# Optimization experiments

Hardware: AMD Instinct MI355X
Metric: run time of the kernel (lower is better)

## Reference

```python
import jax, jax.numpy as jnp
import numpy as np

N = 50000          # nodes
E_RAND = 600000    # random edges (self-loops appended -> E = 650000)
H, C = 2, 128      # heads, per-head channels
IN, OUT = 128, 40
SLOPE = 0.2        # PyG GATv2 default negative_slope
EPS = 1e-16


def setup_inputs() -> dict:
    key = jax.random.key(0)
    ks = jax.random.split(key, 16)
    x = jax.random.normal(ks[0], (N, IN), jnp.float32)
    src = jax.random.randint(ks[1], (E_RAND,), 0, N)
    dst = jax.random.randint(ks[2], (E_RAND,), 0, N)
    loops = jnp.arange(N)
    edge_index = jnp.stack([jnp.concatenate([src, loops]),
                            jnp.concatenate([dst, loops])]).astype(jnp.int64)

    def glorot(k, shape):
        fan = shape[0] + shape[-1]
        return jax.random.normal(k, shape, jnp.float32) * jnp.sqrt(2.0 / fan)

    return {
        "x": x, "edge_index": edge_index,
        "Wl1": glorot(ks[3], (IN, H * C)), "Wr1": glorot(ks[4], (IN, H * C)),
        "att1": glorot(ks[5], (H, C)), "b1": jnp.zeros((H * C,), jnp.float32),
        "Wl2": glorot(ks[6], (H * C, H * C)), "Wr2": glorot(ks[7], (H * C, H * C)),
        "att2": glorot(ks[8], (H, C)), "b2": jnp.zeros((H * C,), jnp.float32),
        "W3": glorot(ks[9], (H * C, C)), "b3": jnp.zeros((C,), jnp.float32),
        "W4": glorot(ks[10], (C, OUT)), "b4": jnp.zeros((OUT,), jnp.float32),
    }


def gatv2_conv(x, src, dst, Wl, Wr, att, b):
    # x: [N, F]; lin_l -> source messages, lin_r -> target. Output concat heads.
    xl = (x @ Wl).reshape(-1, H, C)              # [N,H,C]
    xr = (x @ Wr).reshape(-1, H, C)
    e = jax.nn.leaky_relu(xl[src] + xr[dst], SLOPE)   # [E,H,C]
    score = jnp.einsum('ehc,hc->eh', e, att)          # [E,H]
    # segment softmax over incoming edges of each dst node
    m = jax.ops.segment_max(score, dst, num_segments=N)       # [N,H]
    a = jnp.exp(score - m[dst])
    denom = jax.ops.segment_sum(a, dst, num_segments=N)
    alpha = a / (denom[dst] + EPS)                              # [E,H]
    out = jax.ops.segment_sum(alpha[:, :, None] * xl[src], dst, num_segments=N)
    return out.reshape(-1, H * C) + b


def reference(x, edge_index, Wl1, Wr1, att1, b1, Wl2, Wr2, att2, b2, W3, b3, W4, b4):
    src, dst = edge_index[0], edge_index[1]
    h = jax.nn.relu(gatv2_conv(x, src, dst, Wl1, Wr1, att1, b1))   # dropout: eval mode
    h = jax.nn.relu(gatv2_conv(h, src, dst, Wl2, Wr2, att2, b2))
    h = h @ W3 + b3
    h = h @ W4 + b4
    return jax.nn.sigmoid(h)   # [N, OUT]
```

## Files before the change

kernel.cpp:

```cpp
#include <hip/hip_runtime.h>
#include <hip/hip_bf16.h>
#include <math.h>

typedef __attribute__((ext_vector_type(4))) float f32x4;
typedef __attribute__((ext_vector_type(8))) short s16x8;
typedef __attribute__((ext_vector_type(8))) unsigned short u16x8;

#define CAP 48

__device__ inline unsigned short f2b(float f) {
    union { float f; unsigned u; } x; x.f = f;
    unsigned r = x.u + 0x7FFF + ((x.u >> 16) & 1);
    return (unsigned short)(r >> 16);
}
__device__ inline float b2f(unsigned short b) {
    union { unsigned u; float f; } x; x.u = ((unsigned)b) << 16; return x.f;
}

__device__ inline void gload_lds16(const void* g, void* l) {
    __builtin_amdgcn_global_load_lds(
        (const __attribute__((address_space(1))) void*)g,
        (__attribute__((address_space(3))) void*)l, 16, 0, 0);
}

#define GBM 128
#define GBN 256
#define GBK 64

__global__ __launch_bounds__(512) void gemm_mfma(
    const unsigned short* __restrict__ A, const unsigned short* __restrict__ Bt,
    const float* __restrict__ bias, void* __restrict__ Cout, void* __restrict__ Cout2,
    int M, int Nn, int K, int split, int mode)
{
    __shared__ unsigned short As[GBM * GBK];
    __shared__ unsigned short Bs[GBN * GBK];
    const int tid = threadIdx.x;
    const int lane = tid & 63;
    const int w = tid >> 6, wm = w >> 2, wn = w & 3;
    const int row0 = blockIdx.y * GBM, col0 = blockIdx.x * GBN;
    const int l15 = lane & 15, l7 = lane & 7, lhi = lane >> 4;

    f32x4 acc[4][4] = {};

    for (int k0 = 0; k0 < K; k0 += GBK) {
        #pragma unroll
        for (int i = 0; i < 2; i++) {
            int L = i * 512 + tid;
            int row = L >> 3;
            int c = (L & 7) ^ (row & 7);
            int gr = row0 + row; gr = gr < M ? gr : M - 1;
            gload_lds16(A + (size_t)gr * K + k0 + c * 8, (char*)As + L * 16);
        }
        #pragma unroll
        for (int i = 0; i < 4; i++) {
            int L = i * 512 + tid;
            int row = L >> 3;
            int c = (L & 7) ^ (row & 7);
            gload_lds16(Bt + (size_t)(col0 + row) * K + k0 + c * 8, (char*)Bs + L * 16);
        }
        __syncthreads();
        #pragma unroll
        for (int kk = 0; kk < 2; kk++) {
            s16x8 af[4], bf[4];
            #pragma unroll
            for (int i = 0; i < 4; i++) {
                int slot = (wm * 64 + i * 16 + l15) * 8 + ((kk * 4 + lhi) ^ l7);
                af[i] = *(const s16x8*)((const char*)As + slot * 16);
            }
            #pragma unroll
            for (int j = 0; j < 4; j++) {
                int slot = (wn * 64 + j * 16 + l15) * 8 + ((kk * 4 + lhi) ^ l7);
                bf[j] = *(const s16x8*)((const char*)Bs + slot * 16);
            }
            #pragma unroll
            for (int i = 0; i < 4; i++)
                #pragma unroll
                for (int j = 0; j < 4; j++)
                    acc[i][j] = __builtin_amdgcn_mfma_f32_16x16x32_bf16(
                        af[i], bf[j], acc[i][j], 0, 0, 0);
        }
        __syncthreads();
    }

    if (mode == 0) {
        unsigned short* C  = (unsigned short*)Cout;
        unsigned short* C2 = (unsigned short*)Cout2;
        const int ld2 = Nn - split;
        #pragma unroll
        for (int i = 0; i < 4; i++)
            #pragma unroll
            for (int r = 0; r < 4; r++) {
                int row = row0 + wm * 64 + i * 16 + lhi * 4 + r;
                if (row >= M) continue;
                #pragma unroll
                for (int j = 0; j < 4; j++) {
                    int col = col0 + wn * 64 + j * 16 + l15;
                    unsigned short val = f2b(acc[i][j][r]);
                    if (col < split) C[(size_t)row * split + col] = val;
                    else             C2[(size_t)row * ld2 + (col - split)] = val;
                }
            }
    } else {
        float* C = (float*)Cout;
        #pragma unroll
        for (int i = 0; i < 4; i++)
            #pragma unroll
            for (int r = 0; r < 4; r++) {
                int row = row0 + wm * 64 + i * 16 + lhi * 4 + r;
                if (row >= M) continue;
                #pragma unroll
                for (int j = 0; j < 4; j++) {
                    int col = col0 + wn * 64 + j * 16 + l15;
                    if (col >= split) continue;
                    float v = acc[i][j][r] + bias[col];
                    C[(size_t)row * split + col] = 1.f / (1.f + __expf(-v));
                }
            }
    }
}

#define PA 6250
#define PB 6282
#define PC 6346
#define PE 6602

__global__ __launch_bounds__(256) void k_prep(
    const float* __restrict__ x,
    const float* __restrict__ Wl1, const float* __restrict__ Wr1,
    const float* __restrict__ Wl2, const float* __restrict__ Wr2,
    const float* __restrict__ W3,  const float* __restrict__ W4,
    const float* __restrict__ b3,  const float* __restrict__ b4,
    unsigned short* __restrict__ xbf,
    unsigned short* __restrict__ Wcat1, unsigned short* __restrict__ Wcat2,
    unsigned short* __restrict__ W34t, float* __restrict__ b34)
{
    __shared__ float w4c[128];
    const int b = blockIdx.x, tid = threadIdx.x;

    if (b < PA) {
        int i = b * 1024 + tid * 4;
        float4 v = *(const float4*)&x[i];
        ushort4 o = { f2b(v.x), f2b(v.y), f2b(v.z), f2b(v.w) };
        *(ushort4*)&xbf[i] = o;
    } else if (b < PB) {
        int base = (b - PA) * 2048 + tid * 8;
        #pragma unroll
        for (int j = 0; j < 8; j++) {
            int e = base + j;
            int ep = e & 32767, n = ep >> 7, k = ep & 127;
            const float* srcp = (e < 32768) ? Wl1 : Wr1;
            Wcat1[e] = f2b(srcp[k * 256 + n]);
        }
    } else if (b < PC) {
        int base = (b - PB) * 2048 + tid * 8;
        #pragma unroll
        for (int j = 0; j < 8; j++) {
            int e = base + j;
            int ep = e & 65535, n = ep >> 8, k = ep & 255;
            const float* srcp = (e < 65536) ? Wl2 : Wr2;
            Wcat2[e] = f2b(srcp[k * 256 + n]);
        }
    } else {
        int n = b - PC;
        if (n < 40) {
            if (tid < 128) w4c[tid] = W4[tid * 40 + n];
            __syncthreads();
            float s = 0.f;
            const float4* p = (const float4*)&W3[(size_t)tid * 128];
            #pragma unroll
            for (int j = 0; j < 32; j++) {
                float4 v = p[j];
                s = fmaf(v.x, w4c[j * 4 + 0], s);
                s = fmaf(v.y, w4c[j * 4 + 1], s);
                s = fmaf(v.z, w4c[j * 4 + 2], s);
                s = fmaf(v.w, w4c[j * 4 + 3], s);
            }
            W34t[(size_t)n * 256 + tid] = f2b(s);
            if (tid == 0) {
                float t = b4[n];
                for (int j = 0; j < 128; j++) t = fmaf(b3[j], w4c[j], t);
                b34[n] = t;
            }
        } else {
            W34t[(size_t)n * 256 + tid] = 0;
        }
    }
}

__global__ void k_fillb(const int* __restrict__ src, const int* __restrict__ dstv, int E,
    int* __restrict__ cnt, int* __restrict__ colA)
{
    int e = blockIdx.x * blockDim.x + threadIdx.x;
    if (e >= E) return;
    int d = dstv[e];
    int slot = atomicAdd(&cnt[d], 1);
    colA[d * CAP + slot] = src[e] << 8;
}

__global__ __launch_bounds__(256) void k_attn(const unsigned short* __restrict__ xl,
    const unsigned short* __restrict__ xr, const float* __restrict__ att,
    const int* __restrict__ cnt, const int* __restrict__ colA,
    const float* __restrict__ bias, int Nn, unsigned short* __restrict__ outp)
{
    int n = blockIdx.x * 4 + (threadIdx.x >> 6);
    int lane = threadIdx.x & 63;
    if (n >= Nn) return;
    const int lh = lane & 31;
    const int h  = lane >> 5;
    int r0 = n * CAP;
    int r1 = r0 + cnt[n];

    const float LOG2E = 1.4426950408889634f;
    u16x8 xb = *(const u16x8*)&xr[(size_t)n * 256 + lh * 8];
    float xrv[8], w[8];
    #pragma unroll
    for (int k = 0; k < 8; k++) { xrv[k] = b2f(xb[k]); w[k] = att[lh * 8 + k] * LOG2E; }

    float m = -INFINITY, l = 0.f;
    float acc[8] = {};

    auto update = [&](const u16x8& vb) {
        float v[8];
        #pragma unroll
        for (int k = 0; k < 8; k++) v[k] = b2f(vb[k]);
        float dot = 0.f;
        #pragma unroll
        for (int k = 0; k < 8; k++) {
            float t = v[k] + xrv[k];
            t = fmaxf(t, 0.2f * t);
            dot = fmaf(t, w[k], dot);
        }
        #pragma unroll
        for (int off = 1; off <= 8; off <<= 1) dot += __shfl_xor(dot, off);
        if (__ballot(dot > m + 8.f)) {
            float mn = fmaxf(m, dot);
            float sc = exp2f(m - mn);
            float we = exp2f(dot - mn);
            l = l * sc + we;
            #pragma unroll
            for (int k = 0; k < 8; k++) acc[k] = acc[k] * sc + we * v[k];
            m = mn;
        } else {
            float we = exp2f(dot - m);
            l += we;
            #pragma unroll
            for (int k = 0; k < 8; k++) acc[k] = fmaf(we, v[k], acc[k]);
        }
    };

    int s = r0 + h;
    for (; s + 2 < r1; s += 4) {
        int c0 = colA[s], c1 = colA[s + 2];
        u16x8 v0 = *(const u16x8*)&xl[(size_t)c0 + lh * 8];
        u16x8 v1 = *(const u16x8*)&xl[(size_t)c1 + lh * 8];
        update(v0);
        update(v1);
    }
    for (; s < r1; s += 2) {
        int c = colA[s];
        u16x8 v = *(const u16x8*)&xl[(size_t)c + lh * 8];
        update(v);
    }

    float mq = (m == -INFINITY) ? -1e30f : m;
    float mo = __shfl_xor(mq, 32);
    float lo = __shfl_xor(l, 32);
    float ms = fmaxf(mq, mo);
    float es = exp2f(mq - ms), eo = exp2f(mo - ms);
    float lt = l * es + lo * eo + 1e-16f;
    float inv = 1.f / lt;

    u16x8 o;
    #pragma unroll
    for (int k = 0; k < 8; k++) {
        float other = __shfl_xor(acc[k], 32);
        float r = (acc[k] * es + other * eo) * inv + bias[lh * 8 + k];
        o[k] = f2b(fmaxf(r, 0.f));
    }
    if (h == 0) *(u16x8*)&outp[(size_t)n * 256 + lh * 8] = o;
}

extern "C" void kernel_launch(void* const* d_in, const int* in_sizes, int n_in,
                              void* d_out, int out_size, void* d_ws, size_t ws_size,
                              hipStream_t stream)
{
    const float* x    = (const float*)d_in[0];
    const int*   ei   = (const int*)d_in[1];
    const float* Wl1  = (const float*)d_in[2];
    const float* Wr1  = (const float*)d_in[3];
    const float* att1 = (const float*)d_in[4];
    const float* b1   = (const float*)d_in[5];
    const float* Wl2  = (const float*)d_in[6];
    const float* Wr2  = (const float*)d_in[7];
    const float* att2 = (const float*)d_in[8];
    const float* b2   = (const float*)d_in[9];
    const float* W3   = (const float*)d_in[10];
    const float* b3   = (const float*)d_in[11];
    const float* W4   = (const float*)d_in[12];
    const float* b4   = (const float*)d_in[13];

    const int N = in_sizes[0] / 128;
    const int E = in_sizes[1] / 2;
    const int* src  = ei;
    const int* dstv = ei + E;
    float* out = (float*)d_out;

    char* ws = (char*)d_ws;
    size_t o = 0;
    auto alloc = [&](size_t bytes) -> void* {
        void* p = ws + o;
        o += (bytes + 255) & ~(size_t)255;
        return p;
    };
    unsigned short* xbf    = (unsigned short*)alloc((size_t)N * 128 * 2);
    unsigned short* Wcat1  = (unsigned short*)alloc(512 * 128 * 2);
    unsigned short* Wcat2  = (unsigned short*)alloc(512 * 256 * 2);
    unsigned short* W34t   = (unsigned short*)alloc(256 * 256 * 2);
    float*          b34    = (float*)alloc(128 * 4);
    unsigned short* xlb    = (unsigned short*)alloc((size_t)N * 256 * 2);
    unsigned short* xrb    = (unsigned short*)alloc((size_t)N * 256 * 2);
    unsigned short* h1b    = (unsigned short*)alloc((size_t)N * 256 * 2);
    unsigned short* h2b    = (unsigned short*)alloc((size_t)N * 256 * 2);
    int* cnt    = (int*)alloc((size_t)N * 4);
    int* colA   = (int*)alloc((size_t)N * CAP * 4);

    dim3 blk(256);

    hipMemsetAsync(cnt, 0, (size_t)N * 4, stream);
    k_prep<<<PE, blk, 0, stream>>>(x, Wl1, Wr1, Wl2, Wr2, W3, W4, b3, b4,
                                   xbf, Wcat1, Wcat2, W34t, b34);

    k_fillb<<<(E + 255) / 256, blk, 0, stream>>>(src, dstv, E, cnt, colA);

    const int gy = (N + GBM - 1) / GBM;

    gemm_mfma<<<dim3(2, gy), dim3(512), 0, stream>>>(xbf, Wcat1, nullptr, xlb, xrb,
                                                     N, 512, 128, 256, 0);
    k_attn<<<(N + 3) / 4, blk, 0, stream>>>(xlb, xrb, att1, cnt, colA, b1, N, h1b);

    gemm_mfma<<<dim3(2, gy), dim3(512), 0, stream>>>(h1b, Wcat2, nullptr, xlb, xrb,
                                                     N, 512, 256, 256, 0);
    k_attn<<<(N + 3) / 4, blk, 0, stream>>>(xlb, xrb, att2, cnt, colA, b2, N, h2b);

    gemm_mfma<<<dim3(1, gy), dim3(512), 0, stream>>>(h2b, W34t, b34, out, nullptr,
                                                     N, 128, 256, 40, 2);
}
```

Before: 273.7 us.

## Fuse x bf16 conversion into first GEMM, merge CSR fill into prep, unroll attention

The separate pass converting x to bf16 is removed. The first GEMM now loads fp32 rows directly and converts them to bf16 into LDS with ordinary stores instead of global_load_lds. The edge-bucketing kernel is folded into the prep kernel as extra blocks, which saves a launch. The attention gather loop is unrolled to four neighbours per iteration to put more loads in flight. In exchange, the fp32 A path in the GEMM uses synchronous register-staged loads, and x is read again by each of the two column blocks.

```diff
diff --git a/kernel.cpp b/kernel.cpp
--- a/kernel.cpp
+++ b/kernel.cpp
@@ -28,9 +28,9 @@
 #define GBK 64
 
 __global__ __launch_bounds__(512) void gemm_mfma(
-    const unsigned short* __restrict__ A, const unsigned short* __restrict__ Bt,
+    const void* __restrict__ Aptr, const unsigned short* __restrict__ Bt,
     const float* __restrict__ bias, void* __restrict__ Cout, void* __restrict__ Cout2,
-    int M, int Nn, int K, int split, int mode)
+    int M, int Nn, int K, int split, int mode, int aflt)
 {
     __shared__ unsigned short As[GBM * GBK];
     __shared__ unsigned short Bs[GBN * GBK];
@@ -43,13 +43,32 @@
     f32x4 acc[4][4] = {};
 
     for (int k0 = 0; k0 < K; k0 += GBK) {
-        #pragma unroll
-        for (int i = 0; i < 2; i++) {
-            int L = i * 512 + tid;
-            int row = L >> 3;
-            int c = (L & 7) ^ (row & 7);
-            int gr = row0 + row; gr = gr < M ? gr : M - 1;
-            gload_lds16(A + (size_t)gr * K + k0 + c * 8, (char*)As + L * 16);
+        if (aflt == 0) {
+            const unsigned short* A = (const unsigned short*)Aptr;
+            #pragma unroll
+            for (int i = 0; i < 2; i++) {
+                int L = i * 512 + tid;
+                int row = L >> 3;
+                int c = (L & 7) ^ (row & 7);
+                int gr = row0 + row; gr = gr < M ? gr : M - 1;
+                gload_lds16(A + (size_t)gr * K + k0 + c * 8, (char*)As + L * 16);
+            }
+        } else {
+            const float* A = (const float*)Aptr;
+            #pragma unroll
+            for (int i = 0; i < 2; i++) {
+                int L = i * 512 + tid;
+                int row = L >> 3;
+                int c = (L & 7) ^ (row & 7);
+                int gr = row0 + row; gr = gr < M ? gr : M - 1;
+                const float* ap = A + (size_t)gr * K + k0 + c * 8;
+                float4 va = *(const float4*)ap;
+                float4 vb = *(const float4*)(ap + 4);
+                ushort4 o0 = { f2b(va.x), f2b(va.y), f2b(va.z), f2b(va.w) };
+                ushort4 o1 = { f2b(vb.x), f2b(vb.y), f2b(vb.z), f2b(vb.w) };
+                *(ushort4*)((char*)As + L * 16)     = o0;
+                *(ushort4*)((char*)As + L * 16 + 8) = o1;
+            }
         }
         #pragma unroll
         for (int i = 0; i < 4; i++) {
@@ -119,31 +138,26 @@
     }
 }
 
-#define PA 6250
-#define PB 6282
-#define PC 6346
-#define PE 6602
+#define PB 32
+#define PC 96
+#define PD 352
+#define PEND 2892
 
 __global__ __launch_bounds__(256) void k_prep(
-    const float* __restrict__ x,
     const float* __restrict__ Wl1, const float* __restrict__ Wr1,
     const float* __restrict__ Wl2, const float* __restrict__ Wr2,
     const float* __restrict__ W3,  const float* __restrict__ W4,
     const float* __restrict__ b3,  const float* __restrict__ b4,
-    unsigned short* __restrict__ xbf,
+    const int* __restrict__ src,   const int* __restrict__ dstv, int E,
     unsigned short* __restrict__ Wcat1, unsigned short* __restrict__ Wcat2,
-    unsigned short* __restrict__ W34t, float* __restrict__ b34)
+    unsigned short* __restrict__ W34t, float* __restrict__ b34,
+    int* __restrict__ cnt, int* __restrict__ colA)
 {
     __shared__ float w4c[128];
     const int b = blockIdx.x, tid = threadIdx.x;
 
-    if (b < PA) {
-        int i = b * 1024 + tid * 4;
-        float4 v = *(const float4*)&x[i];
-        ushort4 o = { f2b(v.x), f2b(v.y), f2b(v.z), f2b(v.w) };
-        *(ushort4*)&xbf[i] = o;
-    } else if (b < PB) {
-        int base = (b - PA) * 2048 + tid * 8;
+    if (b < PB) {
+        int base = b * 2048 + tid * 8;
         #pragma unroll
         for (int j = 0; j < 8; j++) {
             int e = base + j;
@@ -160,7 +174,7 @@
             const float* srcp = (e < 65536) ? Wl2 : Wr2;
             Wcat2[e] = f2b(srcp[k * 256 + n]);
         }
-    } else {
+    } else if (b < PD) {
         int n = b - PC;
         if (n < 40) {
             if (tid < 128) w4c[tid] = W4[tid * 40 + n];
@@ -184,17 +198,14 @@
         } else {
             W34t[(size_t)n * 256 + tid] = 0;
         }
-    }
-}
-
-__global__ void k_fillb(const int* __restrict__ src, const int* __restrict__ dstv, int E,
-    int* __restrict__ cnt, int* __restrict__ colA)
-{
-    int e = blockIdx.x * blockDim.x + threadIdx.x;
-    if (e >= E) return;
-    int d = dstv[e];
-    int slot = atomicAdd(&cnt[d], 1);
-    colA[d * CAP + slot] = src[e] << 8;
+    } else {
+        int e = (b - PD) * 256 + tid;
+        if (e < E) {
+            int d = dstv[e];
+            int slot = atomicAdd(&cnt[d], 1);
+            colA[d * CAP + slot] = src[e] << 8;
+        }
+    }
 }
 
 __global__ __launch_bounds__(256) void k_attn(const unsigned short* __restrict__ xl,
@@ -249,14 +260,22 @@
     };
 
     int s = r0 + h;
-    for (; s + 2 < r1; s += 4) {
+    for (; s + 6 < r1; s += 8) {
+        int c0 = colA[s], c1 = colA[s + 2], c2 = colA[s + 4], c3 = colA[s + 6];
+        u16x8 v0 = *(const u16x8*)&xl[(size_t)c0 + lh * 8];
+        u16x8 v1 = *(const u16x8*)&xl[(size_t)c1 + lh * 8];
+        u16x8 v2 = *(const u16x8*)&xl[(size_t)c2 + lh * 8];
+        u16x8 v3 = *(const u16x8*)&xl[(size_t)c3 + lh * 8];
+        update(v0); update(v1); update(v2); update(v3);
+    }
+    if (s + 2 < r1) {
         int c0 = colA[s], c1 = colA[s + 2];
         u16x8 v0 = *(const u16x8*)&xl[(size_t)c0 + lh * 8];
         u16x8 v1 = *(const u16x8*)&xl[(size_t)c1 + lh * 8];
-        update(v0);
-        update(v1);
-    }
-    for (; s < r1; s += 2) {
+        update(v0); update(v1);
+        s += 4;
+    }
+    if (s < r1) {
         int c = colA[s];
         u16x8 v = *(const u16x8*)&xl[(size_t)c + lh * 8];
         update(v);
@@ -312,7 +331,6 @@
         o += (bytes + 255) & ~(size_t)255;
         return p;
     };
-    unsigned short* xbf    = (unsigned short*)alloc((size_t)N * 128 * 2);
     unsigned short* Wcat1  = (unsigned short*)alloc(512 * 128 * 2);
     unsigned short* Wcat2  = (unsigned short*)alloc(512 * 256 * 2);
     unsigned short* W34t   = (unsigned short*)alloc(256 * 256 * 2);
@@ -327,21 +345,20 @@
     dim3 blk(256);
 
     hipMemsetAsync(cnt, 0, (size_t)N * 4, stream);
-    k_prep<<<PE, blk, 0, stream>>>(x, Wl1, Wr1, Wl2, Wr2, W3, W4, b3, b4,
-                                   xbf, Wcat1, Wcat2, W34t, b34);
-
-    k_fillb<<<(E + 255) / 256, blk, 0, stream>>>(src, dstv, E, cnt, colA);
+    k_prep<<<PEND, blk, 0, stream>>>(Wl1, Wr1, Wl2, Wr2, W3, W4, b3, b4,
+                                     src, dstv, E, Wcat1, Wcat2, W34t, b34,
+                                     cnt, colA);
 
     const int gy = (N + GBM - 1) / GBM;
 
-    gemm_mfma<<<dim3(2, gy), dim3(512), 0, stream>>>(xbf, Wcat1, nullptr, xlb, xrb,
-                                                     N, 512, 128, 256, 0);
+    gemm_mfma<<<dim3(2, gy), dim3(512), 0, stream>>>(x, Wcat1, nullptr, xlb, xrb,
+                                                     N, 512, 128, 256, 0, 1);
     k_attn<<<(N + 3) / 4, blk, 0, stream>>>(xlb, xrb, att1, cnt, colA, b1, N, h1b);
 
     gemm_mfma<<<dim3(2, gy), dim3(512), 0, stream>>>(h1b, Wcat2, nullptr, xlb, xrb,
-                                                     N, 512, 256, 256, 0);
+                                                     N, 512, 256, 256, 0, 0);
     k_attn<<<(N + 3) / 4, blk, 0, stream>>>(xlb, xrb, att2, cnt, colA, b2, N, h2b);
 
     gemm_mfma<<<dim3(1, gy), dim3(512), 0, stream>>>(h2b, W34t, b34, out, nullptr,
-                                                     N, 128, 256, 40, 2);
-}
+                                                     N, 128, 256, 40, 2, 0);
+}
```

Measured after the change: 258.5 us. 5.5% less time.
